# Optimization experiments

Hardware: AMD Instinct MI355X
Metric: run time of the kernel (lower is better)

Reference implementation:

```python
import jax, jax.numpy as jnp
import numpy as np
from jax import lax

C = 256

def conv1x1(x, w, b):
    # x: [B,C,H,W], w: [O,C], b: [O]
    return jnp.einsum('bchw,oc->bohw', x, w) + b[None, :, None, None]

def conv3x3_s2(x, w, b):
    # x: [B,C,H,W], w: [O,C,3,3] -> stride 2, pad 1
    y = lax.conv_general_dilated(x, w, window_strides=(2, 2),
                                 padding=((1, 1), (1, 1)),
                                 dimension_numbers=('NCHW', 'OIHW', 'NCHW'))
    return y + b[None, :, None, None]

def to_qv(x):
    # [B,C,H,W] -> permute(0,2,3,1) -> view [B,H,W,1,C]
    return jnp.transpose(x, (0, 2, 3, 1))[:, :, :, None, :]

def to_k(x):
    # [B,C,H,W] -> permute(0,2,3,1) -> view [B,H,W,C,1]
    return jnp.transpose(x, (0, 2, 3, 1))[:, :, :, :, None]

def upsample2x_nearest(x):
    return jnp.repeat(jnp.repeat(x, 2, axis=2), 2, axis=3)


def setup_inputs() -> dict:
    key = jax.random.key(0)
    ks = jax.random.split(key, 20)
    x1 = jax.random.normal(ks[0], (2, C, 128, 128), dtype=jnp.float32)
    x2 = jax.random.normal(ks[1], (2, C, 64, 64), dtype=jnp.float32)
    s = 0.05
    d = {'x1': x1, 'x2': x2}
    names = ['q1', 'q2', 'ks1', 'ks2', 'kup', 'v1', 'v2']
    for i, n in enumerate(names):
        d[n + '_w'] = jax.random.normal(ks[2 + 2 * i], (C, C), dtype=jnp.float32) * s
        d[n + '_b'] = jax.random.normal(ks[3 + 2 * i], (C,), dtype=jnp.float32) * s
    d['kdown_w'] = jax.random.normal(ks[16], (C, C, 3, 3), dtype=jnp.float32) * s
    d['kdown_b'] = jax.random.normal(ks[17], (C,), dtype=jnp.float32) * s
    return d


def reference(x1, x2, q1_w, q1_b, q2_w, q2_b, ks1_w, ks1_b, ks2_w, ks2_b,
              kup_w, kup_b, v1_w, v1_b, v2_w, v2_b, kdown_w, kdown_b):
    q1 = to_qv(conv1x1(x1, q1_w, q1_b))            # [B,128,128,1,C]
    q2 = to_qv(conv1x1(x2, q2_w, q2_b))            # [B,64,64,1,C]
    k_up = to_k(upsample2x_nearest(conv1x1(x2, kup_w, kup_b)))  # [B,128,128,C,1]
    k_self_1 = to_k(conv1x1(x1, ks1_w, ks1_b))     # [B,128,128,C,1]
    k_self_2 = to_k(conv1x1(x2, ks2_w, ks2_b))     # [B,64,64,C,1]
    k_down = to_k(conv3x3_s2(x1, kdown_w, kdown_b))  # [B,64,64,C,1]
    v1 = to_qv(conv1x1(x1, v1_w, v1_b))            # [B,128,128,1,C]
    v2 = to_qv(conv1x1(x2, v2_w, v2_b))            # [B,64,64,1,C]
    return (q1, q2, k_up, k_self_1, k_self_2, k_down, v1, v2)
```

## Files before the change

### kernel.cpp

```cpp
#include <hip/hip_runtime.h>
#include <hip/hip_bf16.h>
#include <stdint.h>


typedef __attribute__((ext_vector_type(8))) __bf16 bf16x8;
typedef __attribute__((ext_vector_type(4))) float f32x4;
typedef __attribute__((ext_vector_type(8))) unsigned short u16x8;

typedef const __attribute__((address_space(1))) uint32_t* gptr_t;
typedef __attribute__((address_space(3))) uint32_t* lptr_t;

__device__ __forceinline__ void cp16(void* lds, const void* g) {
  gptr_t gp = reinterpret_cast<gptr_t>(reinterpret_cast<uintptr_t>(g));
  lptr_t lp = reinterpret_cast<lptr_t>(
      static_cast<uint32_t>(reinterpret_cast<uintptr_t>(lds)));
  __builtin_amdgcn_global_load_lds(gp, lp, 16, 0, 0);
}

struct WArgs {
  const float* w1[7];
  const float* kdw;
};

__global__ void prep(WArgs a, uint16_t* __restrict__ wf,
                     uint16_t* __restrict__ x1p) {
  const int bx = blockIdx.x;
  if (bx < 512) {
    const int idx = bx * 256 + threadIdx.x;
    const int mat = idx >> 13;
    const int g = idx & 8191;
    const int jg = g >> 9;
    const int kc = (g >> 6) & 7;
    const int lane = g & 63;
    const int o = jg * 16 + (lane & 15);
    const int k0 = kc * 32 + (lane >> 4) * 8;
    float f[8];
    if (mat < 7) {
      const float* w = a.w1[mat];
      const float4 v0 = *(const float4*)(w + o * 256 + k0);
      const float4 v1 = *(const float4*)(w + o * 256 + k0 + 4);
      f[0] = v0.x; f[1] = v0.y; f[2] = v0.z; f[3] = v0.w;
      f[4] = v1.x; f[5] = v1.y; f[6] = v1.z; f[7] = v1.w;
    } else {
      const int tap = mat - 7;
#pragma unroll
      for (int e = 0; e < 8; e++)
        f[e] = a.kdw[(long)o * 2304 + (long)(k0 + e) * 9 + tap];
    }
    u16x8 u;
#pragma unroll
    for (int e = 0; e < 8; e++) {
      __hip_bfloat16 hb = __float2bfloat16(f[e]);
      u[e] = *reinterpret_cast<uint16_t*>(&hb);
    }
    *(u16x8*)(wf + (long)idx * 8) = u;
  } else {
    const int c = (bx - 512) * 256 + threadIdx.x;
    const int b = (c >= 16512) ? 1 : 0;
    const int cc = c - b * 16512;
    int h, w, g8;
    if (cc < 4160) {
      h = 0; w = cc >> 5; g8 = cc & 31;
    } else if (cc < 8320) {
      const int s = cc - 4160; h = 129; w = s >> 5; g8 = s & 31;
    } else if (cc < 12416) {
      const int s = cc - 8320; h = 1 + (s >> 5); w = 0; g8 = s & 31;
    } else {
      const int s = cc - 12416; h = 1 + (s >> 5); w = 129; g8 = s & 31;
    }
    u16x8 z = {};
    *(u16x8*)(x1p + (((long)(b * 130 + h)) * 130 + w) * 256 + g8 * 8) = z;
  }
}

__global__ void transpose_all(const float* __restrict__ x1,
                              const float* __restrict__ x2,
                              uint16_t* __restrict__ x1p,
                              uint16_t* __restrict__ x2b) {
  const float* src;
  uint16_t* dst;
  int H, W, pad, b, h;
  if ((int)blockIdx.z < 256) {
    src = x1; dst = x1p; H = 128; W = 128; pad = 1;
    b = blockIdx.z >> 7; h = blockIdx.z & 127;
  } else {
    if (blockIdx.x) return;
    const int t = blockIdx.z - 256;
    src = x2; dst = x2b; H = 64; W = 64; pad = 0;
    b = t >> 6; h = t & 63;
  }
  __shared__ float tile[64][65];
  const int tid = threadIdx.x;
  const int wt = blockIdx.x * 64;
  const int ct = blockIdx.y * 64;
  const long cs = (long)H * W;
  const float* s = src + ((long)(b * 256 + ct) * H + h) * W + wt;
  const int rw = tid >> 4;
  const int rf = tid & 15;
#pragma unroll
  for (int p = 0; p < 4; p++) {
    const int cl = p * 16 + rw;
    const float4 v = *(const float4*)(s + (long)cl * cs + rf * 4);
    tile[cl][rf * 4 + 0] = v.x;
    tile[cl][rf * 4 + 1] = v.y;
    tile[cl][rf * 4 + 2] = v.z;
    tile[cl][rf * 4 + 3] = v.w;
  }
  __syncthreads();
  const int wl0 = tid >> 3;
  const int cg = tid & 7;
  const int Wp = W + 2 * pad;
  const long rowb = ((long)(b * (H + 2 * pad) + h + pad)) * Wp + pad + wt;
#pragma unroll
  for (int p = 0; p < 2; p++) {
    const int wl = p * 32 + wl0;
    u16x8 u;
#pragma unroll
    for (int k = 0; k < 8; k++) {
      __hip_bfloat16 hb = __float2bfloat16(tile[cg * 8 + k][wl]);
      u[k] = *reinterpret_cast<uint16_t*>(&hb);
    }
    *(u16x8*)(dst + (rowb + wl) * 256 + ct + cg * 8) = u;
  }
}

struct Job {
  const uint16_t* A;
  const uint16_t* Wf;
  const float* bias;
  float* out;
  int start;
  int mode;
};
struct JobArgs {
  Job j[8];
};

__global__ __launch_bounds__(256, 2) void fused_gemm(JobArgs args) {
  int jid = 0;
#pragma unroll
  for (int t = 1; t < 8; t++)
    if ((int)blockIdx.x >= args.j[t].start) jid = t;
  const Job jb = args.j[jid];
  const int bid = blockIdx.x - jb.start;
  const int mode = jb.mode;

  __shared__ __align__(16) uint16_t lA[32768];

  const int tid = threadIdx.x;
  const int lane = tid & 63;
  const int wave = tid >> 6;
  const int wr = wave & 1;
  const int wc = wave >> 1;
  const int q = lane >> 4;
  const int l15 = lane & 15;

  if (mode == 3) {
    const int mtile = bid >> 1;
    const int ntile = bid & 1;
    const int row = mtile * 64 + wave * 16 + (lane >> 2);
    const long p =
        ((long)((row >> 12) * 130 + 2 * ((row >> 6) & 63))) * 130 + 2 * (row & 63);
    const uint16_t* rowA = jb.A + p * 256 + (lane & 3) * 8;

    f32x4 acc[2][4] = {};
    for (int tap = 0; tap < 9; tap++) {
      const int kh = tap / 3;
      const int kw = tap - kh * 3;
      const long aoff = (long)(kh * 130 + kw) * 256;
      const uint16_t* wf = jb.Wf + (long)tap * 65536;
      if (tap) __syncthreads();
#pragma unroll
      for (int kap = 0; kap < 8; kap++)
        cp16(lA + (kap * 256 + wave * 64) * 8, rowA + aoff + kap * 32);
      __syncthreads();
#pragma unroll
      for (int kc = 0; kc < 8; kc++) {
        bf16x8 av[2];
#pragma unroll
        for (int i = 0; i < 2; i++)
          av[i] = *(const bf16x8*)(lA + (kc * 64 + wr * 32 + i * 16 + l15) * 32 + q * 8);
#pragma unroll
        for (int j = 0; j < 4; j++) {
          const bf16x8 bv = *(const bf16x8*)(
              wf + ((long)((ntile * 8 + wc * 4 + j) * 8 + kc) * 64 + lane) * 8);
#pragma unroll
          for (int i = 0; i < 2; i++)
            acc[i][j] = __builtin_amdgcn_mfma_f32_16x16x32_bf16(av[i], bv,
                                                                acc[i][j], 0, 0, 0);
        }
      }
    }
    const int nb = ntile * 128 + wc * 64 + l15;
    const int mb = mtile * 64 + wr * 32 + q * 4;
#pragma unroll
    for (int j = 0; j < 4; j++) {
      const int n = nb + j * 16;
      const float bvs = jb.bias[n];
#pragma unroll
      for (int i = 0; i < 2; i++) {
        const int m0 = mb + i * 16;
#pragma unroll
        for (int r = 0; r < 4; r++)
          jb.out[(long)(m0 + r) * 256 + n] = acc[i][j][r] + bvs;
      }
    }
    return;
  }

  const int mtile = bid;
  const uint16_t* rowA[2];
  {
    const int rbase = wave * 16 + (lane >> 2);
#pragma unroll
    for (int rh = 0; rh < 2; rh++) {
      const int m = mtile * 128 + rh * 64 + rbase;
      long p;
      if (mode == 0) {
        p = ((long)((m >> 14) * 130 + ((m >> 7) & 127) + 1)) * 130 + (m & 127) + 1;
      } else {
        p = m;
      }
      rowA[rh] = jb.A + p * 256 + (lane & 3) * 8;
    }
  }

#pragma unroll
  for (int kap = 0; kap < 16; kap++)
    cp16(lA + (kap * 256 + wave * 64) * 8, rowA[kap & 1] + (kap >> 1) * 32);
  __syncthreads();

  f32x4 acc[4][8] = {};
#pragma unroll
  for (int kc = 0; kc < 8; kc++) {
    bf16x8 av[4];
#pragma unroll
    for (int i = 0; i < 4; i++)
      av[i] = *(const bf16x8*)(lA + (kc * 128 + wr * 64 + i * 16 + l15) * 32 + q * 8);
#pragma unroll
    for (int j = 0; j < 8; j++) {
      const bf16x8 bv =
          *(const bf16x8*)(jb.Wf + ((long)((wc * 8 + j) * 8 + kc) * 64 + lane) * 8);
#pragma unroll
      for (int i = 0; i < 4; i++)
        acc[i][j] = __builtin_amdgcn_mfma_f32_16x16x32_bf16(av[i], bv,
                                                            acc[i][j], 0, 0, 0);
    }
  }

  const int nb = wc * 128 + l15;
  const int mb = mtile * 128 + wr * 64 + q * 4;
  if (mode == 2) {
#pragma unroll
    for (int j = 0; j < 8; j++) {
      const int n = nb + j * 16;
      const float bvs = jb.bias[n];
#pragma unroll
      for (int i = 0; i < 4; i++) {
        const int m0 = mb + i * 16;
#pragma unroll
        for (int r = 0; r < 4; r++) {
          const int m = m0 + r;
          const int b = m >> 12;
          const int h2 = (m >> 6) & 63;
          const int w2 = m & 63;
          const float val = acc[i][j][r] + bvs;
          float* o =
              jb.out + ((long)(b * 128 + 2 * h2) * 128 + 2 * w2) * 256 + n;
          o[0] = val;
          o[256] = val;
          o[32768] = val;
          o[32768 + 256] = val;
        }
      }
    }
  } else {
#pragma unroll
    for (int j = 0; j < 8; j++) {
      const int n = nb + j * 16;
      const float bvs = jb.bias[n];
#pragma unroll
      for (int i = 0; i < 4; i++) {
        const int m0 = mb + i * 16;
#pragma unroll
        for (int r = 0; r < 4; r++)
          jb.out[(long)(m0 + r) * 256 + n] = acc[i][j][r] + bvs;
      }
    }
  }
}

extern "C" void kernel_launch(void* const* d_in, const int* in_sizes, int n_in,
                              void* d_out, int out_size, void* d_ws,
                              size_t ws_size, hipStream_t stream) {
  (void)in_sizes; (void)n_in; (void)out_size; (void)ws_size;
  const float* x1 = (const float*)d_in[0];
  const float* x2 = (const float*)d_in[1];
  float* out = (float*)d_out;

  uint16_t* x1p = (uint16_t*)d_ws;
  uint16_t* x2b = x1p + 8652800;
  uint16_t* wf = x2b + 2097152;

  WArgs wa;
  wa.w1[0] = (const float*)d_in[2];
  wa.w1[1] = (const float*)d_in[4];
  wa.w1[2] = (const float*)d_in[6];
  wa.w1[3] = (const float*)d_in[8];
  wa.w1[4] = (const float*)d_in[10];
  wa.w1[5] = (const float*)d_in[12];
  wa.w1[6] = (const float*)d_in[14];
  wa.kdw = (const float*)d_in[16];
  prep<<<641, 256, 0, stream>>>(wa, wf, x1p);
  transpose_all<<<dim3(2, 4, 384), 256, 0, stream>>>(x1, x2, x1p, x2b);

  JobArgs ja;
  ja.j[0] = {x1p, wf + 7 * 65536, (const float*)d_in[17], out + 29360128L, 0,    3};
  ja.j[1] = {x1p, wf + 0 * 65536, (const float*)d_in[3],  out + 0L,        256,  0};
  ja.j[2] = {x1p, wf + 2 * 65536, (const float*)d_in[7],  out + 18874368L, 512,  0};
  ja.j[3] = {x1p, wf + 5 * 65536, (const float*)d_in[13], out + 31457280L, 768,  0};
  ja.j[4] = {x2b, wf + 4 * 65536, (const float*)d_in[11], out + 10485760L, 1024, 2};
  ja.j[5] = {x2b, wf + 1 * 65536, (const float*)d_in[5],  out + 8388608L,  1088, 1};
  ja.j[6] = {x2b, wf + 3 * 65536, (const float*)d_in[9],  out + 27262976L, 1152, 1};
  ja.j[7] = {x2b, wf + 6 * 65536, (const float*)d_in[15], out + 39845888L, 1216, 1};
  fused_gemm<<<1280, 256, 0, stream>>>(ja);
}
```

Baseline: 295.9 us.

## Merge prep and transpose kernels; use 512-thread GEMM blocks with swizzled LDS

Folds the weight-prep/pad-zeroing kernel and the activation transpose into a single launch, removing one kernel launch and its gap. The GEMM moves to 512-thread blocks (8 waves), each covering the full 256-wide N so activation tiles are loaded once instead of per N-half for the strided conv. A quadrant XOR swizzle is applied to the LDS layout to cut bank conflicts on the A-fragment reads. Per-wave accumulators shrink, which raises occupancy pressure from the launch bounds, and the job offsets are reworked to match.

```diff
diff --git a/kernel.cpp b/kernel.cpp
--- a/kernel.cpp
+++ b/kernel.cpp
@@ -22,11 +22,16 @@
   const float* kdw;
 };
 
-__global__ void prep(WArgs a, uint16_t* __restrict__ wf,
-                     uint16_t* __restrict__ x1p) {
+__global__ void prep_transpose(WArgs a, const float* __restrict__ x1,
+                               const float* __restrict__ x2,
+                               uint16_t* __restrict__ wf,
+                               uint16_t* __restrict__ x1p,
+                               uint16_t* __restrict__ x2b) {
+  __shared__ float tile[64][65];
   const int bx = blockIdx.x;
+  const int tid = threadIdx.x;
   if (bx < 512) {
-    const int idx = bx * 256 + threadIdx.x;
+    const int idx = bx * 256 + tid;
     const int mat = idx >> 13;
     const int g = idx & 8191;
     const int jg = g >> 9;
@@ -54,8 +59,10 @@
       u[e] = *reinterpret_cast<uint16_t*>(&hb);
     }
     *(u16x8*)(wf + (long)idx * 8) = u;
-  } else {
-    const int c = (bx - 512) * 256 + threadIdx.x;
+    return;
+  }
+  if (bx < 641) {
+    const int c = (bx - 512) * 256 + tid;
     const int b = (c >= 16512) ? 1 : 0;
     const int cc = c - b * 16512;
     int h, w, g8;
@@ -70,29 +77,25 @@
     }
     u16x8 z = {};
     *(u16x8*)(x1p + (((long)(b * 130 + h)) * 130 + w) * 256 + g8 * 8) = z;
-  }
-}
-
-__global__ void transpose_all(const float* __restrict__ x1,
-                              const float* __restrict__ x2,
-                              uint16_t* __restrict__ x1p,
-                              uint16_t* __restrict__ x2b) {
+    return;
+  }
+  const int t = bx - 641;
   const float* src;
   uint16_t* dst;
-  int H, W, pad, b, h;
-  if ((int)blockIdx.z < 256) {
+  int H, W, pad, b, h, bxx, by;
+  if (t < 2048) {
     src = x1; dst = x1p; H = 128; W = 128; pad = 1;
-    b = blockIdx.z >> 7; h = blockIdx.z & 127;
+    bxx = t & 1; by = (t >> 1) & 3;
+    const int z = t >> 3; b = z >> 7; h = z & 127;
   } else {
-    if (blockIdx.x) return;
-    const int t = blockIdx.z - 256;
+    const int t2 = t - 2048;
     src = x2; dst = x2b; H = 64; W = 64; pad = 0;
-    b = t >> 6; h = t & 63;
-  }
-  __shared__ float tile[64][65];
-  const int tid = threadIdx.x;
-  const int wt = blockIdx.x * 64;
-  const int ct = blockIdx.y * 64;
+    bxx = 0; by = t2 & 3;
+    const int z = t2 >> 2;
+    b = z >> 6; h = z & 63;
+  }
+  const int wt = bxx * 64;
+  const int ct = by * 64;
   const long cs = (long)H * W;
   const float* s = src + ((long)(b * 256 + ct) * H + h) * W + wt;
   const int rw = tid >> 4;
@@ -136,7 +139,7 @@
   Job j[8];
 };
 
-__global__ __launch_bounds__(256, 2) void fused_gemm(JobArgs args) {
+__global__ __launch_bounds__(512, 4) void fused_gemm(JobArgs args) {
   int jid = 0;
 #pragma unroll
   for (int t = 1; t < 8; t++)
@@ -150,18 +153,19 @@
   const int tid = threadIdx.x;
   const int lane = tid & 63;
   const int wave = tid >> 6;
-  const int wr = wave & 1;
-  const int wc = wave >> 1;
+  const int wr = wave >> 2;
+  const int wc = wave & 3;
   const int q = lane >> 4;
   const int l15 = lane & 15;
+  const int ksel = ((lane & 3) ^ ((lane >> 3) & 3)) * 8;
+  const int qsw = (q ^ ((l15 >> 1) & 3)) * 8;
 
   if (mode == 3) {
-    const int mtile = bid >> 1;
-    const int ntile = bid & 1;
-    const int row = mtile * 64 + wave * 16 + (lane >> 2);
+    const int mtile = bid;
+    const int row = mtile * 64 + wc * 16 + (lane >> 2);
     const long p =
         ((long)((row >> 12) * 130 + 2 * ((row >> 6) & 63))) * 130 + 2 * (row & 63);
-    const uint16_t* rowA = jb.A + p * 256 + (lane & 3) * 8;
+    const uint16_t* rowA = jb.A + p * 256 + wr * 32 + ksel;
 
     f32x4 acc[2][4] = {};
     for (int tap = 0; tap < 9; tap++) {
@@ -171,19 +175,19 @@
       const uint16_t* wf = jb.Wf + (long)tap * 65536;
       if (tap) __syncthreads();
 #pragma unroll
-      for (int kap = 0; kap < 8; kap++)
-        cp16(lA + (kap * 256 + wave * 64) * 8, rowA + aoff + kap * 32);
+      for (int kap = 0; kap < 4; kap++)
+        cp16(lA + kap * 4096 + wave * 512, rowA + aoff + kap * 64);
       __syncthreads();
 #pragma unroll
       for (int kc = 0; kc < 8; kc++) {
         bf16x8 av[2];
 #pragma unroll
         for (int i = 0; i < 2; i++)
-          av[i] = *(const bf16x8*)(lA + (kc * 64 + wr * 32 + i * 16 + l15) * 32 + q * 8);
+          av[i] = *(const bf16x8*)(lA + (kc * 64 + wr * 32 + i * 16 + l15) * 32 + qsw);
 #pragma unroll
         for (int j = 0; j < 4; j++) {
           const bf16x8 bv = *(const bf16x8*)(
-              wf + ((long)((ntile * 8 + wc * 4 + j) * 8 + kc) * 64 + lane) * 8);
+              wf + ((long)(((wc * 4 + j) * 8 + kc) * 64 + lane)) * 8);
 #pragma unroll
           for (int i = 0; i < 2; i++)
             acc[i][j] = __builtin_amdgcn_mfma_f32_16x16x32_bf16(av[i], bv,
@@ -191,7 +195,7 @@
         }
       }
     }
-    const int nb = ntile * 128 + wc * 64 + l15;
+    const int nb = wc * 64 + l15;
     const int mb = mtile * 64 + wr * 32 + q * 4;
 #pragma unroll
     for (int j = 0; j < 4; j++) {
@@ -209,38 +213,32 @@
   }
 
   const int mtile = bid;
-  const uint16_t* rowA[2];
   {
-    const int rbase = wave * 16 + (lane >> 2);
-#pragma unroll
-    for (int rh = 0; rh < 2; rh++) {
-      const int m = mtile * 128 + rh * 64 + rbase;
-      long p;
-      if (mode == 0) {
-        p = ((long)((m >> 14) * 130 + ((m >> 7) & 127) + 1)) * 130 + (m & 127) + 1;
-      } else {
-        p = m;
-      }
-      rowA[rh] = jb.A + p * 256 + (lane & 3) * 8;
-    }
-  }
-
-#pragma unroll
-  for (int kap = 0; kap < 16; kap++)
-    cp16(lA + (kap * 256 + wave * 64) * 8, rowA[kap & 1] + (kap >> 1) * 32);
+    const int m = mtile * 128 + wave * 16 + (lane >> 2);
+    long p;
+    if (mode == 0) {
+      p = ((long)((m >> 14) * 130 + ((m >> 7) & 127) + 1)) * 130 + (m & 127) + 1;
+    } else {
+      p = m;
+    }
+    const uint16_t* rowA = jb.A + p * 256 + ksel;
+#pragma unroll
+    for (int kap = 0; kap < 8; kap++)
+      cp16(lA + kap * 4096 + wave * 512, rowA + kap * 32);
+  }
   __syncthreads();
 
-  f32x4 acc[4][8] = {};
+  f32x4 acc[4][4] = {};
 #pragma unroll
   for (int kc = 0; kc < 8; kc++) {
     bf16x8 av[4];
 #pragma unroll
     for (int i = 0; i < 4; i++)
-      av[i] = *(const bf16x8*)(lA + (kc * 128 + wr * 64 + i * 16 + l15) * 32 + q * 8);
-#pragma unroll
-    for (int j = 0; j < 8; j++) {
-      const bf16x8 bv =
-          *(const bf16x8*)(jb.Wf + ((long)((wc * 8 + j) * 8 + kc) * 64 + lane) * 8);
+      av[i] = *(const bf16x8*)(lA + (kc * 128 + wr * 64 + i * 16 + l15) * 32 + qsw);
+#pragma unroll
+    for (int j = 0; j < 4; j++) {
+      const bf16x8 bv = *(const bf16x8*)(
+          jb.Wf + ((long)(((wc * 4 + j) * 8 + kc) * 64 + lane)) * 8);
 #pragma unroll
       for (int i = 0; i < 4; i++)
         acc[i][j] = __builtin_amdgcn_mfma_f32_16x16x32_bf16(av[i], bv,
@@ -248,11 +246,11 @@
     }
   }
 
-  const int nb = wc * 128 + l15;
+  const int nb = wc * 64 + l15;
   const int mb = mtile * 128 + wr * 64 + q * 4;
   if (mode == 2) {
 #pragma unroll
-    for (int j = 0; j < 8; j++) {
+    for (int j = 0; j < 4; j++) {
       const int n = nb + j * 16;
       const float bvs = jb.bias[n];
 #pragma unroll
@@ -276,7 +274,7 @@
     }
   } else {
 #pragma unroll
-    for (int j = 0; j < 8; j++) {
+    for (int j = 0; j < 4; j++) {
       const int n = nb + j * 16;
       const float bvs = jb.bias[n];
 #pragma unroll
@@ -311,17 +309,16 @@
   wa.w1[5] = (const float*)d_in[12];
   wa.w1[6] = (const float*)d_in[14];
   wa.kdw = (const float*)d_in[16];
-  prep<<<641, 256, 0, stream>>>(wa, wf, x1p);
-  transpose_all<<<dim3(2, 4, 384), 256, 0, stream>>>(x1, x2, x1p, x2b);
+  prep_transpose<<<3201, 256, 0, stream>>>(wa, x1, x2, wf, x1p, x2b);
 
   JobArgs ja;
   ja.j[0] = {x1p, wf + 7 * 65536, (const float*)d_in[17], out + 29360128L, 0,    3};
-  ja.j[1] = {x1p, wf + 0 * 65536, (const float*)d_in[3],  out + 0L,        256,  0};
-  ja.j[2] = {x1p, wf + 2 * 65536, (const float*)d_in[7],  out + 18874368L, 512,  0};
-  ja.j[3] = {x1p, wf + 5 * 65536, (const float*)d_in[13], out + 31457280L, 768,  0};
-  ja.j[4] = {x2b, wf + 4 * 65536, (const float*)d_in[11], out + 10485760L, 1024, 2};
-  ja.j[5] = {x2b, wf + 1 * 65536, (const float*)d_in[5],  out + 8388608L,  1088, 1};
-  ja.j[6] = {x2b, wf + 3 * 65536, (const float*)d_in[9],  out + 27262976L, 1152, 1};
-  ja.j[7] = {x2b, wf + 6 * 65536, (const float*)d_in[15], out + 39845888L, 1216, 1};
-  fused_gemm<<<1280, 256, 0, stream>>>(ja);
+  ja.j[1] = {x1p, wf + 0 * 65536, (const float*)d_in[3],  out + 0L,        128,  0};
+  ja.j[2] = {x1p, wf + 2 * 65536, (const float*)d_in[7],  out + 18874368L, 384,  0};
+  ja.j[3] = {x1p, wf + 5 * 65536, (const float*)d_in[13], out + 31457280L, 640,  0};
+  ja.j[4] = {x2b, wf + 4 * 65536, (const float*)d_in[11], out + 10485760L, 896,  2};
+  ja.j[5] = {x2b, wf + 1 * 65536, (const float*)d_in[5],  out + 8388608L,  960,  1};
+  ja.j[6] = {x2b, wf + 3 * 65536, (const float*)d_in[9],  out + 27262976L, 1024, 1};
+  ja.j[7] = {x2b, wf + 6 * 65536, (const float*)d_in[15], out + 39845888L, 1088, 1};
+  fused_gemm<<<1152, 512, 0, stream>>>(ja);
 }
```

Result: slower. 329.3 us (+11.3%).

## Merge prep and transpose kernels and XOR-swizzle LDS A tile layout

Applied to the files above, without the earlier changes.

Combines the weight-prep/pad-zeroing kernel with the activation transpose kernel into one launch, dropping the idle x2 blocks the old grid produced. It also XOR-swizzles which 16-byte K chunk each lane copies into LDS and applies the matching swizzle when reading A fragments, to reduce LDS bank conflicts in the MFMA loop. The merged kernel always reserves the transpose tile's shared memory, even in blocks that do not use it.

```diff
diff --git a/kernel.cpp b/kernel.cpp
--- a/kernel.cpp
+++ b/kernel.cpp
@@ -22,11 +22,16 @@
   const float* kdw;
 };
 
-__global__ void prep(WArgs a, uint16_t* __restrict__ wf,
-                     uint16_t* __restrict__ x1p) {
+__global__ void prep_transpose(WArgs a, const float* __restrict__ x1,
+                               const float* __restrict__ x2,
+                               uint16_t* __restrict__ wf,
+                               uint16_t* __restrict__ x1p,
+                               uint16_t* __restrict__ x2b) {
+  __shared__ float tile[64][65];
   const int bx = blockIdx.x;
+  const int tid = threadIdx.x;
   if (bx < 512) {
-    const int idx = bx * 256 + threadIdx.x;
+    const int idx = bx * 256 + tid;
     const int mat = idx >> 13;
     const int g = idx & 8191;
     const int jg = g >> 9;
@@ -54,8 +59,10 @@
       u[e] = *reinterpret_cast<uint16_t*>(&hb);
     }
     *(u16x8*)(wf + (long)idx * 8) = u;
-  } else {
-    const int c = (bx - 512) * 256 + threadIdx.x;
+    return;
+  }
+  if (bx < 641) {
+    const int c = (bx - 512) * 256 + tid;
     const int b = (c >= 16512) ? 1 : 0;
     const int cc = c - b * 16512;
     int h, w, g8;
@@ -70,29 +77,25 @@
     }
     u16x8 z = {};
     *(u16x8*)(x1p + (((long)(b * 130 + h)) * 130 + w) * 256 + g8 * 8) = z;
-  }
-}
-
-__global__ void transpose_all(const float* __restrict__ x1,
-                              const float* __restrict__ x2,
-                              uint16_t* __restrict__ x1p,
-                              uint16_t* __restrict__ x2b) {
+    return;
+  }
+  const int t = bx - 641;
   const float* src;
   uint16_t* dst;
-  int H, W, pad, b, h;
-  if ((int)blockIdx.z < 256) {
+  int H, W, pad, b, h, bxx, by;
+  if (t < 2048) {
     src = x1; dst = x1p; H = 128; W = 128; pad = 1;
-    b = blockIdx.z >> 7; h = blockIdx.z & 127;
+    bxx = t & 1; by = (t >> 1) & 3;
+    const int z = t >> 3; b = z >> 7; h = z & 127;
   } else {
-    if (blockIdx.x) return;
-    const int t = blockIdx.z - 256;
+    const int t2 = t - 2048;
     src = x2; dst = x2b; H = 64; W = 64; pad = 0;
-    b = t >> 6; h = t & 63;
-  }
-  __shared__ float tile[64][65];
-  const int tid = threadIdx.x;
-  const int wt = blockIdx.x * 64;
-  const int ct = blockIdx.y * 64;
+    bxx = 0; by = t2 & 3;
+    const int z = t2 >> 2;
+    b = z >> 6; h = z & 63;
+  }
+  const int wt = bxx * 64;
+  const int ct = by * 64;
   const long cs = (long)H * W;
   const float* s = src + ((long)(b * 256 + ct) * H + h) * W + wt;
   const int rw = tid >> 4;
@@ -154,6 +157,8 @@
   const int wc = wave >> 1;
   const int q = lane >> 4;
   const int l15 = lane & 15;
+  const int ksel = ((lane & 3) ^ ((lane >> 3) & 3)) * 8;
+  const int qsw = (q ^ ((l15 >> 1) & 3)) * 8;
 
   if (mode == 3) {
     const int mtile = bid >> 1;
@@ -161,7 +166,7 @@
     const int row = mtile * 64 + wave * 16 + (lane >> 2);
     const long p =
         ((long)((row >> 12) * 130 + 2 * ((row >> 6) & 63))) * 130 + 2 * (row & 63);
-    const uint16_t* rowA = jb.A + p * 256 + (lane & 3) * 8;
+    const uint16_t* rowA = jb.A + p * 256 + ksel;
 
     f32x4 acc[2][4] = {};
     for (int tap = 0; tap < 9; tap++) {
@@ -179,7 +184,7 @@
         bf16x8 av[2];
 #pragma unroll
         for (int i = 0; i < 2; i++)
-          av[i] = *(const bf16x8*)(lA + (kc * 64 + wr * 32 + i * 16 + l15) * 32 + q * 8);
+          av[i] = *(const bf16x8*)(lA + (kc * 64 + wr * 32 + i * 16 + l15) * 32 + qsw);
 #pragma unroll
         for (int j = 0; j < 4; j++) {
           const bf16x8 bv = *(const bf16x8*)(
@@ -221,7 +226,7 @@
       } else {
         p = m;
       }
-      rowA[rh] = jb.A + p * 256 + (lane & 3) * 8;
+      rowA[rh] = jb.A + p * 256 + ksel;
     }
   }
 
@@ -236,7 +241,7 @@
     bf16x8 av[4];
 #pragma unroll
     for (int i = 0; i < 4; i++)
-      av[i] = *(const bf16x8*)(lA + (kc * 128 + wr * 64 + i * 16 + l15) * 32 + q * 8);
+      av[i] = *(const bf16x8*)(lA + (kc * 128 + wr * 64 + i * 16 + l15) * 32 + qsw);
 #pragma unroll
     for (int j = 0; j < 8; j++) {
       const bf16x8 bv =
@@ -311,8 +316,7 @@
   wa.w1[5] = (const float*)d_in[12];
   wa.w1[6] = (const float*)d_in[14];
   wa.kdw = (const float*)d_in[16];
-  prep<<<641, 256, 0, stream>>>(wa, wf, x1p);
-  transpose_all<<<dim3(2, 4, 384), 256, 0, stream>>>(x1, x2, x1p, x2b);
+  prep_transpose<<<3201, 256, 0, stream>>>(wa, x1, x2, wf, x1p, x2b);
 
   JobArgs ja;
   ja.j[0] = {x1p, wf + 7 * 65536, (const float*)d_in[17], out + 29360128L, 0,    3};
```

Result: no change. 291.5 us (-1.5%).
